# Kernel tuning notes

Measured on AMD Instinct MI355X. Metric: run time of the kernel, lower is better.

The kernel has to match this reference:

```python
import jax, jax.numpy as jnp
import numpy as np

N = 1_000_000
B = 64            # number of point clouds (segments)
IN_DIM = 3
HID = 128
AFF = 16
AH = 64           # agent hidden
AL = 32           # agent latent
AA = 8            # agent action


def setup_inputs() -> dict:
    key = jax.random.key(0)
    ks = jax.random.split(key, 20)
    s = 0.05
    inp = {
        "pos": jax.random.normal(ks[0], (N, IN_DIM), jnp.float32),
        "batch": jnp.sort(jax.random.randint(ks[1], (N,), 0, B, jnp.int32)),
        "agent_h": jnp.zeros((B, AH), jnp.float32),
        "coherence_signal_prev": jnp.zeros((B, 1), jnp.float32),
        "coherence_spatial_prev": jnp.zeros((N,), jnp.float32),
        # FunctorF params (3 -> 128 -> 16)
        "Wf1": jax.random.normal(ks[2], (IN_DIM, HID), jnp.float32) * s,
        "bf1": jnp.zeros((HID,), jnp.float32),
        "Wf2": jax.random.normal(ks[3], (HID, AFF), jnp.float32) * s,
        "bf2": jnp.zeros((AFF,), jnp.float32),
        # FunctorG params (16 -> 128 -> 3)
        "Wg1": jax.random.normal(ks[4], (AFF, HID), jnp.float32) * s,
        "bg1": jnp.zeros((HID,), jnp.float32),
        "Wg2": jax.random.normal(ks[5], (HID, IN_DIM), jnp.float32) * s,
        "bg2": jnp.zeros((IN_DIM,), jnp.float32),
        # AgentC GRU cell (obs=16 -> h=64) + latent/action heads
        "Wx": jax.random.normal(ks[6], (AFF, 3 * AH), jnp.float32) * s,
        "Wh": jax.random.normal(ks[7], (AH, 3 * AH), jnp.float32) * s,
        "bx": jnp.zeros((3 * AH,), jnp.float32),
        "bh": jnp.zeros((3 * AH,), jnp.float32),
        "Wlat": jax.random.normal(ks[8], (AH, AL), jnp.float32) * s,
        "blat": jnp.zeros((AL,), jnp.float32),
        "Wact": jax.random.normal(ks[9], (AL, AA), jnp.float32) * s,
        "bact": jnp.zeros((AA,), jnp.float32),
    }
    return inp


def _segment_mean(x, seg, num_segments):
    # x: (N, ...) float; seg: (N,) int. Mean over each segment (empty -> 0).
    sums = jax.ops.segment_sum(x, seg, num_segments=num_segments)
    counts = jax.ops.segment_sum(jnp.ones_like(seg, x.dtype), seg, num_segments=num_segments)
    denom = jnp.maximum(counts, 1.0)
    return sums / (denom[:, None] if x.ndim > 1 else denom)


def _forward(pos, batch, agent_h, Wf1, bf1, Wf2, bf2, Wg1, bg1, Wg2, bg2,
             Wx, Wh, bx, bh, Wlat, blat, Wact, bact):
    # F: Shape -> Affordance (per-point MLP)
    affordances = jax.nn.relu(pos @ Wf1 + bf1) @ Wf2 + bf2              # (N, AFF)
    # G: Affordance -> Shape reconstruction
    reconstructed_pos = jax.nn.relu(affordances @ Wg1 + bg1) @ Wg2 + bg2  # (N, 3)
    # Coherence (eta): per-point squared error, segment-mean per cloud
    point_errors = jnp.sum((pos - reconstructed_pos) ** 2, axis=-1)     # (N,)
    coherence_signal = _segment_mean(point_errors, batch, B)[:, None]   # (B, 1)
    coherence_spatial = point_errors                                    # (N,)
    # Segment-mean pooled affordances per cloud
    batch_affordances = _segment_mean(affordances, batch, B)            # (B, AFF)
    # AgentC: GRU cell + latent/action heads
    gx = batch_affordances @ Wx + bx                                    # (B, 3*AH)
    gh = agent_h @ Wh + bh                                              # (B, 3*AH)
    gx_r, gx_z, gx_n = jnp.split(gx, 3, axis=-1)
    gh_r, gh_z, gh_n = jnp.split(gh, 3, axis=-1)
    r = jax.nn.sigmoid(gx_r + gh_r)
    z = jax.nn.sigmoid(gx_z + gh_z)
    n = jnp.tanh(gx_n + r * gh_n)
    agent_h_next = (1.0 - z) * n + z * agent_h                          # (B, AH)
    latent = jnp.tanh(agent_h_next @ Wlat + blat)                       # (B, AL)
    agent_action = latent @ Wact + bact                                 # (B, AA)
    return (affordances, reconstructed_pos, coherence_signal,
            coherence_spatial, agent_action, agent_h_next)


def reference(pos, batch, agent_h, coherence_signal_prev, coherence_spatial_prev,
              Wf1, bf1, Wf2, bf2, Wg1, bg1, Wg2, bg2,
              Wx, Wh, bx, bh, Wlat, blat, Wact, bact):
    # coherence_*_prev are part of the original interface but unused in the math.
    return _forward(pos, batch, agent_h, Wf1, bf1, Wf2, bf2, Wg1, bg1, Wg2, bg2,
                    Wx, Wh, bx, bh, Wlat, blat, Wact, bact)
```

## Files before the change

kernel.cpp:

```cpp
#include <hip/hip_runtime.h>
#include <stdint.h>

#define N_PTS 1000000
#define B_SEG 64
#define HID 128
#define AFFD 16
#define AH 64
#define AL 32
#define AA 8

#define TPB 256
#define NT 8
#define PTS_WAVE (16 * NT)
#define PTS_BLK (PTS_WAVE * 4)
#define MAX_REP 8

#define O_AFF 0
#define O_REC (16 * N_PTS)
#define O_SIG (19 * N_PTS)
#define O_SPA (19 * N_PTS + B_SEG)
#define O_ACT (20 * N_PTS + B_SEG)
#define O_HN  (20 * N_PTS + B_SEG + B_SEG * AA)


typedef __attribute__((ext_vector_type(8))) short bf16x8;
typedef __attribute__((ext_vector_type(4))) float f32x4;

static __device__ __forceinline__ short f2bf(float f) {
  __bf16 b = (__bf16)f;
  return __builtin_bit_cast(short, b);
}

__global__ __launch_bounds__(TPB, 1) void point_kernel(
    const float* __restrict__ pos, const int* __restrict__ batch,
    const float* __restrict__ Wf1, const float* __restrict__ bf1v,
    const float* __restrict__ Wf2, const float* __restrict__ bf2v,
    const float* __restrict__ Wg1, const float* __restrict__ bg1v,
    const float* __restrict__ Wg2, const float* __restrict__ bg2v,
    float* __restrict__ out, float* __restrict__ ws, int rep) {
  const int lane = threadIdx.x & 63;
  const int wid = threadIdx.x >> 6;
  const int m = lane & 15;
  const int q = lane >> 4;
  const int wbase = blockIdx.x * PTS_BLK + wid * PTS_WAVE;
  float* __restrict__ wsr = ws + (size_t)(blockIdx.x % rep) * (B_SEG * 18);

  bf16x8 Af1[8], Ag1[8], Af2[4], Ag2[4];
#pragma unroll
  for (int jb = 0; jb < 8; jb++) {
    const int j = jb * 16 + m;
    bf16x8 a = {0, 0, 0, 0, 0, 0, 0, 0};
    if (q == 0) {
      a[0] = f2bf(Wf1[0 * HID + j]);
      a[1] = f2bf(Wf1[1 * HID + j]);
      a[2] = f2bf(Wf1[2 * HID + j]);
      a[3] = f2bf(bf1v[j]);
    }
    Af1[jb] = a;
    bf16x8 g = {0, 0, 0, 0, 0, 0, 0, 0};
#pragma unroll
    for (int e = 0; e < 4; e++) g[e] = f2bf(Wg1[(4 * q + e) * HID + j]);
    if (q == 0) g[4] = f2bf(bg1v[j]);
    Ag1[jb] = g;
  }
#pragma unroll
  for (int kb = 0; kb < 4; kb++) {
    bf16x8 a2, g2;
#pragma unroll
    for (int e = 0; e < 8; e++) {
      const int j = kb * 32 + 4 * q + (e & 3) + 16 * (e >> 2);
      a2[e] = f2bf(Wf2[j * AFFD + m]);
      g2[e] = (m < 3) ? f2bf(Wg2[j * 3 + m]) : (short)0;
    }
    Af2[kb] = a2;
    Ag2[kb] = g2;
  }
  const float bf2r0 = bf2v[4 * q + 0], bf2r1 = bf2v[4 * q + 1];
  const float bf2r2 = bf2v[4 * q + 2], bf2r3 = bf2v[4 * q + 3];
  const float bg20 = bg2v[0], bg21 = bg2v[1], bg22 = bg2v[2];
  const short one = (short)0x3F80;
  const f32x4 zf = {0.f, 0.f, 0.f, 0.f};

  int cur = -1, cntT = 0;
  float acc0 = 0.f, acc1 = 0.f, acc2 = 0.f, acc3 = 0.f, accE = 0.f;

  auto flush = [&]() {
    float r0 = acc0, r1 = acc1, r2 = acc2, r3 = acc3, re = accE;
#pragma unroll
    for (int msk = 1; msk <= 8; msk <<= 1) {
      r0 += __shfl_xor(r0, msk);
      r1 += __shfl_xor(r1, msk);
      r2 += __shfl_xor(r2, msk);
      r3 += __shfl_xor(r3, msk);
      re += __shfl_xor(re, msk);
    }
    if (m == 0) {
      float* wp = wsr + cur * 18;
      atomicAdd(wp + 2 + 4 * q + 0, r0);
      atomicAdd(wp + 2 + 4 * q + 1, r1);
      atomicAdd(wp + 2 + 4 * q + 2, r2);
      atomicAdd(wp + 2 + 4 * q + 3, r3);
      if (q == 0) {
        atomicAdd(wp + 0, re);
        atomicAdd(wp + 1, 16.f * (float)cntT);
      }
    }
    acc0 = acc1 = acc2 = acc3 = accE = 0.f;
    cntT = 0;
  };

  auto do_pair = [&](int pt0, float (&aa)[2][4], float (&ee)[2], int (&sgv)[2],
                     bool (&vv)[2]) {
    float X[2], Y[2], Z[2];
    bf16x8 Bp[2];
#pragma unroll
    for (int u = 0; u < 2; u++) {
      const int p = pt0 + 16 * u + m;
      vv[u] = (p < N_PTS);
      const int pc = vv[u] ? p : (N_PTS - 1);
      X[u] = pos[pc * 3 + 0];
      Y[u] = pos[pc * 3 + 1];
      Z[u] = pos[pc * 3 + 2];
      sgv[u] = batch[pc];
      bf16x8 b = {0, 0, 0, 0, 0, 0, 0, 0};
      if (q == 0) {
        b[0] = f2bf(X[u]);
        b[1] = f2bf(Y[u]);
        b[2] = f2bf(Z[u]);
        b[3] = one;
      }
      Bp[u] = b;
    }

    bf16x8 Bh[2][4];
#pragma unroll
    for (int u = 0; u < 2; u++)
#pragma unroll
      for (int kb = 0; kb < 4; kb++) {
        f32x4 c0 = __builtin_amdgcn_mfma_f32_16x16x32_bf16(Af1[2 * kb + 0], Bp[u], zf, 0, 0, 0);
        f32x4 c1 = __builtin_amdgcn_mfma_f32_16x16x32_bf16(Af1[2 * kb + 1], Bp[u], zf, 0, 0, 0);
        bf16x8 b;
        b[0] = f2bf(fmaxf(c0[0], 0.f));
        b[1] = f2bf(fmaxf(c0[1], 0.f));
        b[2] = f2bf(fmaxf(c0[2], 0.f));
        b[3] = f2bf(fmaxf(c0[3], 0.f));
        b[4] = f2bf(fmaxf(c1[0], 0.f));
        b[5] = f2bf(fmaxf(c1[1], 0.f));
        b[6] = f2bf(fmaxf(c1[2], 0.f));
        b[7] = f2bf(fmaxf(c1[3], 0.f));
        Bh[u][kb] = b;
      }

    bf16x8 Ba[2];
#pragma unroll
    for (int u = 0; u < 2; u++) {
      f32x4 c01 = __builtin_amdgcn_mfma_f32_16x16x32_bf16(Af2[0], Bh[u][0], zf, 0, 0, 0);
      c01 = __builtin_amdgcn_mfma_f32_16x16x32_bf16(Af2[1], Bh[u][1], c01, 0, 0, 0);
      f32x4 c23 = __builtin_amdgcn_mfma_f32_16x16x32_bf16(Af2[2], Bh[u][2], zf, 0, 0, 0);
      c23 = __builtin_amdgcn_mfma_f32_16x16x32_bf16(Af2[3], Bh[u][3], c23, 0, 0, 0);
      aa[u][0] = c01[0] + c23[0] + bf2r0;
      aa[u][1] = c01[1] + c23[1] + bf2r1;
      aa[u][2] = c01[2] + c23[2] + bf2r2;
      aa[u][3] = c01[3] + c23[3] + bf2r3;
      bf16x8 b;
      b[0] = f2bf(aa[u][0]);
      b[1] = f2bf(aa[u][1]);
      b[2] = f2bf(aa[u][2]);
      b[3] = f2bf(aa[u][3]);
      b[4] = one;
      b[5] = 0;
      b[6] = 0;
      b[7] = 0;
      Ba[u] = b;
    }

    bf16x8 Bh2[2][4];
#pragma unroll
    for (int u = 0; u < 2; u++)
#pragma unroll
      for (int kb = 0; kb < 4; kb++) {
        f32x4 c0 = __builtin_amdgcn_mfma_f32_16x16x32_bf16(Ag1[2 * kb + 0], Ba[u], zf, 0, 0, 0);
        f32x4 c1 = __builtin_amdgcn_mfma_f32_16x16x32_bf16(Ag1[2 * kb + 1], Ba[u], zf, 0, 0, 0);
        bf16x8 b;
        b[0] = f2bf(fmaxf(c0[0], 0.f));
        b[1] = f2bf(fmaxf(c0[1], 0.f));
        b[2] = f2bf(fmaxf(c0[2], 0.f));
        b[3] = f2bf(fmaxf(c0[3], 0.f));
        b[4] = f2bf(fmaxf(c1[0], 0.f));
        b[5] = f2bf(fmaxf(c1[1], 0.f));
        b[6] = f2bf(fmaxf(c1[2], 0.f));
        b[7] = f2bf(fmaxf(c1[3], 0.f));
        Bh2[u][kb] = b;
      }

#pragma unroll
    for (int u = 0; u < 2; u++) {
      f32x4 c01 = __builtin_amdgcn_mfma_f32_16x16x32_bf16(Ag2[0], Bh2[u][0], zf, 0, 0, 0);
      c01 = __builtin_amdgcn_mfma_f32_16x16x32_bf16(Ag2[1], Bh2[u][1], c01, 0, 0, 0);
      f32x4 c23 = __builtin_amdgcn_mfma_f32_16x16x32_bf16(Ag2[2], Bh2[u][2], zf, 0, 0, 0);
      c23 = __builtin_amdgcn_mfma_f32_16x16x32_bf16(Ag2[3], Bh2[u][3], c23, 0, 0, 0);

      float err = 0.f, rc0 = 0.f, rc1 = 0.f, rc2 = 0.f;
      if (q == 0) {
        rc0 = c01[0] + c23[0] + bg20;
        rc1 = c01[1] + c23[1] + bg21;
        rc2 = c01[2] + c23[2] + bg22;
        const float dx = X[u] - rc0, dy = Y[u] - rc1, dz = Z[u] - rc2;
        err = fmaf(dx, dx, fmaf(dy, dy, dz * dz));
      }
      ee[u] = err;

      if (vv[u]) {
        const int p = pt0 + 16 * u + m;
        float4 st;
        st.x = aa[u][0]; st.y = aa[u][1]; st.z = aa[u][2]; st.w = aa[u][3];
        *(float4*)(out + O_AFF + (size_t)p * 16 + 4 * q) = st;
        if (q == 0) {
          float* orc = out + O_REC + (size_t)p * 3;
          orc[0] = rc0; orc[1] = rc1; orc[2] = rc2;
          out[O_SPA + p] = err;
        }
      }
    }
  };

  const int cA = (wbase < N_PTS) ? wbase : (N_PTS - 1);
  const int cB = (wbase + PTS_WAVE - 1 < N_PTS) ? (wbase + PTS_WAVE - 1) : (N_PTS - 1);
  const int segFirst = batch[cA];
  const bool wave_clean = (wbase + PTS_WAVE <= N_PTS) && (segFirst == batch[cB]);

  float aa[2][4];
  float ee[2];
  int sgv[2];
  bool vv[2];

  if (wave_clean) {
#pragma unroll 1
    for (int tt = 0; tt < NT; tt += 2) {
      do_pair(wbase + tt * 16, aa, ee, sgv, vv);
      acc0 += aa[0][0] + aa[1][0];
      acc1 += aa[0][1] + aa[1][1];
      acc2 += aa[0][2] + aa[1][2];
      acc3 += aa[0][3] + aa[1][3];
      accE += ee[0] + ee[1];
    }
    cur = segFirst;
    cntT = NT;
    flush();
  } else {
#pragma unroll 1
    for (int tt = 0; tt < NT; tt += 2) {
      do_pair(wbase + tt * 16, aa, ee, sgv, vv);
#pragma unroll
      for (int u = 0; u < 2; u++) {
        const int pt0u = wbase + (tt + u) * 16;
        const int useg = __shfl(sgv[u], 0);
        const bool cln = __all(sgv[u] == useg) && (pt0u + 16 <= N_PTS);
        if (cln && useg == cur) {
          acc0 += aa[u][0]; acc1 += aa[u][1];
          acc2 += aa[u][2]; acc3 += aa[u][3];
          accE += ee[u];
          cntT++;
        } else {
          if (cntT > 0) flush();
          if (cln) {
            cur = useg;
            acc0 = aa[u][0]; acc1 = aa[u][1];
            acc2 = aa[u][2]; acc3 = aa[u][3];
            accE = ee[u];
            cntT = 1;
          } else {
            cur = -1;
            if (vv[u]) {
              float* wp = wsr + sgv[u] * 18;
              atomicAdd(wp + 2 + 4 * q + 0, aa[u][0]);
              atomicAdd(wp + 2 + 4 * q + 1, aa[u][1]);
              atomicAdd(wp + 2 + 4 * q + 2, aa[u][2]);
              atomicAdd(wp + 2 + 4 * q + 3, aa[u][3]);
              if (q == 0) {
                atomicAdd(wp + 0, ee[u]);
                atomicAdd(wp + 1, 1.f);
              }
            }
          }
        }
      }
    }
    if (cntT > 0) flush();
  }
}

__global__ __launch_bounds__(64) void agent_kernel(
    const float* __restrict__ ws, int rep, const float* __restrict__ agent_h,
    const float* __restrict__ Wx, const float* __restrict__ Wh,
    const float* __restrict__ bx, const float* __restrict__ bh,
    const float* __restrict__ Wlat, const float* __restrict__ blat,
    const float* __restrict__ Wact, const float* __restrict__ bact,
    float* __restrict__ out) {
  const int b = blockIdx.x;
  const int t = threadIdx.x;
  __shared__ float sAff[AFFD];
  __shared__ float sHn[AH];
  __shared__ float sLat[AL];

  float errs = 0.f, cnts = 0.f, affs = 0.f;
  for (int r = 0; r < rep; r++) {
    const float* wp = ws + ((size_t)r * B_SEG + b) * 18;
    errs += wp[0];
    cnts += wp[1];
    if (t < AFFD) affs += wp[2 + t];
  }
  const float cnt = fmaxf(cnts, 1.f);
  if (t == 0) out[O_SIG + b] = errs / cnt;
  if (t < AFFD) sAff[t] = affs / cnt;
  const float h_prev = agent_h[b * AH + t];
  __syncthreads();

  float pr  = bx[t] + bh[t];
  float pz  = bx[64 + t] + bh[64 + t];
  float pnx = bx[128 + t];
  float pnh = bh[128 + t];
#pragma unroll
  for (int k = 0; k < AFFD; k++) {
    const float a = sAff[k];
    pr  = fmaf(a, Wx[k * 192 + t], pr);
    pz  = fmaf(a, Wx[k * 192 + 64 + t], pz);
    pnx = fmaf(a, Wx[k * 192 + 128 + t], pnx);
  }
#pragma unroll
  for (int k = 0; k < AH; k++) {
    const float h = __shfl(h_prev, k);
    pr  = fmaf(h, Wh[k * 192 + t], pr);
    pz  = fmaf(h, Wh[k * 192 + 64 + t], pz);
    pnh = fmaf(h, Wh[k * 192 + 128 + t], pnh);
  }
  const float r = 1.f / (1.f + expf(-pr));
  const float z = 1.f / (1.f + expf(-pz));
  const float n = tanhf(pnx + r * pnh);
  const float hn = fmaf(1.f - z, n, z * h_prev);
  sHn[t] = hn;
  out[O_HN + b * AH + t] = hn;
  __syncthreads();

  if (t < AL) {
    float acc = blat[t];
#pragma unroll
    for (int k = 0; k < AH; k++) acc = fmaf(sHn[k], Wlat[k * AL + t], acc);
    sLat[t] = tanhf(acc);
  }
  __syncthreads();

  if (t < AA) {
    float acc = bact[t];
#pragma unroll
    for (int k = 0; k < AL; k++) acc = fmaf(sLat[k], Wact[k * AA + t], acc);
    out[O_ACT + b * AA + t] = acc;
  }
}

extern "C" void kernel_launch(void* const* d_in, const int* in_sizes, int n_in,
                              void* d_out, int out_size, void* d_ws, size_t ws_size,
                              hipStream_t stream) {
  const float* pos     = (const float*)d_in[0];
  const int*   batch   = (const int*)d_in[1];
  const float* agent_h = (const float*)d_in[2];
  const float* Wf1  = (const float*)d_in[5];
  const float* bf1v = (const float*)d_in[6];
  const float* Wf2  = (const float*)d_in[7];
  const float* bf2v = (const float*)d_in[8];
  const float* Wg1  = (const float*)d_in[9];
  const float* bg1v = (const float*)d_in[10];
  const float* Wg2  = (const float*)d_in[11];
  const float* bg2v = (const float*)d_in[12];
  const float* Wx   = (const float*)d_in[13];
  const float* Wh   = (const float*)d_in[14];
  const float* bx   = (const float*)d_in[15];
  const float* bh   = (const float*)d_in[16];
  const float* Wlat = (const float*)d_in[17];
  const float* blat = (const float*)d_in[18];
  const float* Wact = (const float*)d_in[19];
  const float* bact = (const float*)d_in[20];
  float* out = (float*)d_out;
  float* ws = (float*)d_ws;

  const size_t one_rep = (size_t)B_SEG * 18 * sizeof(float);
  int rep = (int)(ws_size / one_rep);
  if (rep > MAX_REP) rep = MAX_REP;
  if (rep < 1) rep = 1;

  hipMemsetAsync(ws, 0, (size_t)rep * one_rep, stream);

  const int nblk = (N_PTS + PTS_BLK - 1) / PTS_BLK;
  point_kernel<<<nblk, TPB, 0, stream>>>(pos, batch, Wf1, bf1v, Wf2, bf2v,
                                         Wg1, bg1v, Wg2, bg2v, out, ws, rep);
  agent_kernel<<<B_SEG, 64, 0, stream>>>(ws, rep, agent_h, Wx, Wh, bx, bh,
                                         Wlat, blat, Wact, bact, out);
}
```

Measured before the change: 228.4 us.

## Add unrolled clean-wave path with register double-buffered position prefetch

For waves whose points all belong to one segment, a dedicated fully unrolled path now prefetches the next pair of point positions into a second register buffer while the current pair runs through the MFMA chain. It also skips the per-point batch loads and segment checks on that path. The launch bound is raised to allow two blocks per CU, which tightens the register budget. The extra prefetch registers and full unrolling under that tighter budget risk spills.

```diff
diff --git a/kernel.cpp b/kernel.cpp
--- a/kernel.cpp
+++ b/kernel.cpp
@@ -31,7 +31,7 @@
   return __builtin_bit_cast(short, b);
 }
 
-__global__ __launch_bounds__(TPB, 1) void point_kernel(
+__global__ __launch_bounds__(TPB, 2) void point_kernel(
     const float* __restrict__ pos, const int* __restrict__ batch,
     const float* __restrict__ Wf1, const float* __restrict__ bf1v,
     const float* __restrict__ Wf2, const float* __restrict__ bf2v,
@@ -108,6 +108,147 @@
     acc0 = acc1 = acc2 = acc3 = accE = 0.f;
     cntT = 0;
   };
+
+  const int cA = (wbase < N_PTS) ? wbase : (N_PTS - 1);
+  const int cB = (wbase + PTS_WAVE - 1 < N_PTS) ? (wbase + PTS_WAVE - 1) : (N_PTS - 1);
+  const int segFirst = batch[cA];
+  const bool wave_clean = (wbase + PTS_WAVE <= N_PTS) && (segFirst == batch[cB]);
+
+  if (wave_clean) {
+    float Xb[2][2], Yb[2][2], Zb[2][2];
+#pragma unroll
+    for (int u = 0; u < 2; u++) {
+      const int p = wbase + 16 * u + m;
+      Xb[0][u] = pos[p * 3 + 0];
+      Yb[0][u] = pos[p * 3 + 1];
+      Zb[0][u] = pos[p * 3 + 2];
+    }
+
+#pragma unroll
+    for (int pp = 0; pp < NT / 2; pp++) {
+      const int cr = pp & 1, nx = cr ^ 1;
+      if (pp + 1 < NT / 2) {
+#pragma unroll
+        for (int u = 0; u < 2; u++) {
+          const int p = wbase + (pp + 1) * 32 + 16 * u + m;
+          Xb[nx][u] = pos[p * 3 + 0];
+          Yb[nx][u] = pos[p * 3 + 1];
+          Zb[nx][u] = pos[p * 3 + 2];
+        }
+      }
+
+      bf16x8 Bp[2];
+#pragma unroll
+      for (int u = 0; u < 2; u++) {
+        bf16x8 b = {0, 0, 0, 0, 0, 0, 0, 0};
+        if (q == 0) {
+          b[0] = f2bf(Xb[cr][u]);
+          b[1] = f2bf(Yb[cr][u]);
+          b[2] = f2bf(Zb[cr][u]);
+          b[3] = one;
+        }
+        Bp[u] = b;
+      }
+
+      bf16x8 Bh[2][4];
+#pragma unroll
+      for (int u = 0; u < 2; u++)
+#pragma unroll
+        for (int kb = 0; kb < 4; kb++) {
+          f32x4 c0 = __builtin_amdgcn_mfma_f32_16x16x32_bf16(Af1[2 * kb + 0], Bp[u], zf, 0, 0, 0);
+          f32x4 c1 = __builtin_amdgcn_mfma_f32_16x16x32_bf16(Af1[2 * kb + 1], Bp[u], zf, 0, 0, 0);
+          bf16x8 b;
+          b[0] = f2bf(fmaxf(c0[0], 0.f));
+          b[1] = f2bf(fmaxf(c0[1], 0.f));
+          b[2] = f2bf(fmaxf(c0[2], 0.f));
+          b[3] = f2bf(fmaxf(c0[3], 0.f));
+          b[4] = f2bf(fmaxf(c1[0], 0.f));
+          b[5] = f2bf(fmaxf(c1[1], 0.f));
+          b[6] = f2bf(fmaxf(c1[2], 0.f));
+          b[7] = f2bf(fmaxf(c1[3], 0.f));
+          Bh[u][kb] = b;
+        }
+
+      float aa[2][4];
+      bf16x8 Ba[2];
+#pragma unroll
+      for (int u = 0; u < 2; u++) {
+        f32x4 c01 = __builtin_amdgcn_mfma_f32_16x16x32_bf16(Af2[0], Bh[u][0], zf, 0, 0, 0);
+        c01 = __builtin_amdgcn_mfma_f32_16x16x32_bf16(Af2[1], Bh[u][1], c01, 0, 0, 0);
+        f32x4 c23 = __builtin_amdgcn_mfma_f32_16x16x32_bf16(Af2[2], Bh[u][2], zf, 0, 0, 0);
+        c23 = __builtin_amdgcn_mfma_f32_16x16x32_bf16(Af2[3], Bh[u][3], c23, 0, 0, 0);
+        aa[u][0] = c01[0] + c23[0] + bf2r0;
+        aa[u][1] = c01[1] + c23[1] + bf2r1;
+        aa[u][2] = c01[2] + c23[2] + bf2r2;
+        aa[u][3] = c01[3] + c23[3] + bf2r3;
+        bf16x8 b;
+        b[0] = f2bf(aa[u][0]);
+        b[1] = f2bf(aa[u][1]);
+        b[2] = f2bf(aa[u][2]);
+        b[3] = f2bf(aa[u][3]);
+        b[4] = one;
+        b[5] = 0;
+        b[6] = 0;
+        b[7] = 0;
+        Ba[u] = b;
+      }
+
+      bf16x8 Bh2[2][4];
+#pragma unroll
+      for (int u = 0; u < 2; u++)
+#pragma unroll
+        for (int kb = 0; kb < 4; kb++) {
+          f32x4 c0 = __builtin_amdgcn_mfma_f32_16x16x32_bf16(Ag1[2 * kb + 0], Ba[u], zf, 0, 0, 0);
+          f32x4 c1 = __builtin_amdgcn_mfma_f32_16x16x32_bf16(Ag1[2 * kb + 1], Ba[u], zf, 0, 0, 0);
+          bf16x8 b;
+          b[0] = f2bf(fmaxf(c0[0], 0.f));
+          b[1] = f2bf(fmaxf(c0[1], 0.f));
+          b[2] = f2bf(fmaxf(c0[2], 0.f));
+          b[3] = f2bf(fmaxf(c0[3], 0.f));
+          b[4] = f2bf(fmaxf(c1[0], 0.f));
+          b[5] = f2bf(fmaxf(c1[1], 0.f));
+          b[6] = f2bf(fmaxf(c1[2], 0.f));
+          b[7] = f2bf(fmaxf(c1[3], 0.f));
+          Bh2[u][kb] = b;
+        }
+
+#pragma unroll
+      for (int u = 0; u < 2; u++) {
+        f32x4 c01 = __builtin_amdgcn_mfma_f32_16x16x32_bf16(Ag2[0], Bh2[u][0], zf, 0, 0, 0);
+        c01 = __builtin_amdgcn_mfma_f32_16x16x32_bf16(Ag2[1], Bh2[u][1], c01, 0, 0, 0);
+        f32x4 c23 = __builtin_amdgcn_mfma_f32_16x16x32_bf16(Ag2[2], Bh2[u][2], zf, 0, 0, 0);
+        c23 = __builtin_amdgcn_mfma_f32_16x16x32_bf16(Ag2[3], Bh2[u][3], c23, 0, 0, 0);
+
+        float err = 0.f, rc0 = 0.f, rc1 = 0.f, rc2 = 0.f;
+        if (q == 0) {
+          rc0 = c01[0] + c23[0] + bg20;
+          rc1 = c01[1] + c23[1] + bg21;
+          rc2 = c01[2] + c23[2] + bg22;
+          const float dx = Xb[cr][u] - rc0, dy = Yb[cr][u] - rc1, dz = Zb[cr][u] - rc2;
+          err = fmaf(dx, dx, fmaf(dy, dy, dz * dz));
+        }
+        acc0 += aa[u][0];
+        acc1 += aa[u][1];
+        acc2 += aa[u][2];
+        acc3 += aa[u][3];
+        accE += err;
+
+        const int p = wbase + pp * 32 + 16 * u + m;
+        float4 st;
+        st.x = aa[u][0]; st.y = aa[u][1]; st.z = aa[u][2]; st.w = aa[u][3];
+        *(float4*)(out + O_AFF + (size_t)p * 16 + 4 * q) = st;
+        if (q == 0) {
+          float* orc = out + O_REC + (size_t)p * 3;
+          orc[0] = rc0; orc[1] = rc1; orc[2] = rc2;
+          out[O_SPA + p] = err;
+        }
+      }
+    }
+    cur = segFirst;
+    cntT = NT;
+    flush();
+    return;
+  }
 
   auto do_pair = [&](int pt0, float (&aa)[2][4], float (&ee)[2], int (&sgv)[2],
                      bool (&vv)[2]) {
@@ -224,70 +365,49 @@
     }
   };
 
-  const int cA = (wbase < N_PTS) ? wbase : (N_PTS - 1);
-  const int cB = (wbase + PTS_WAVE - 1 < N_PTS) ? (wbase + PTS_WAVE - 1) : (N_PTS - 1);
-  const int segFirst = batch[cA];
-  const bool wave_clean = (wbase + PTS_WAVE <= N_PTS) && (segFirst == batch[cB]);
-
   float aa[2][4];
   float ee[2];
   int sgv[2];
   bool vv[2];
-
-  if (wave_clean) {
 #pragma unroll 1
-    for (int tt = 0; tt < NT; tt += 2) {
-      do_pair(wbase + tt * 16, aa, ee, sgv, vv);
-      acc0 += aa[0][0] + aa[1][0];
-      acc1 += aa[0][1] + aa[1][1];
-      acc2 += aa[0][2] + aa[1][2];
-      acc3 += aa[0][3] + aa[1][3];
-      accE += ee[0] + ee[1];
-    }
-    cur = segFirst;
-    cntT = NT;
-    flush();
-  } else {
-#pragma unroll 1
-    for (int tt = 0; tt < NT; tt += 2) {
-      do_pair(wbase + tt * 16, aa, ee, sgv, vv);
-#pragma unroll
-      for (int u = 0; u < 2; u++) {
-        const int pt0u = wbase + (tt + u) * 16;
-        const int useg = __shfl(sgv[u], 0);
-        const bool cln = __all(sgv[u] == useg) && (pt0u + 16 <= N_PTS);
-        if (cln && useg == cur) {
-          acc0 += aa[u][0]; acc1 += aa[u][1];
-          acc2 += aa[u][2]; acc3 += aa[u][3];
-          accE += ee[u];
-          cntT++;
+  for (int tt = 0; tt < NT; tt += 2) {
+    do_pair(wbase + tt * 16, aa, ee, sgv, vv);
+#pragma unroll
+    for (int u = 0; u < 2; u++) {
+      const int pt0u = wbase + (tt + u) * 16;
+      const int useg = __shfl(sgv[u], 0);
+      const bool cln = __all(sgv[u] == useg) && (pt0u + 16 <= N_PTS);
+      if (cln && useg == cur) {
+        acc0 += aa[u][0]; acc1 += aa[u][1];
+        acc2 += aa[u][2]; acc3 += aa[u][3];
+        accE += ee[u];
+        cntT++;
+      } else {
+        if (cntT > 0) flush();
+        if (cln) {
+          cur = useg;
+          acc0 = aa[u][0]; acc1 = aa[u][1];
+          acc2 = aa[u][2]; acc3 = aa[u][3];
+          accE = ee[u];
+          cntT = 1;
         } else {
-          if (cntT > 0) flush();
-          if (cln) {
-            cur = useg;
-            acc0 = aa[u][0]; acc1 = aa[u][1];
-            acc2 = aa[u][2]; acc3 = aa[u][3];
-            accE = ee[u];
-            cntT = 1;
-          } else {
-            cur = -1;
-            if (vv[u]) {
-              float* wp = wsr + sgv[u] * 18;
-              atomicAdd(wp + 2 + 4 * q + 0, aa[u][0]);
-              atomicAdd(wp + 2 + 4 * q + 1, aa[u][1]);
-              atomicAdd(wp + 2 + 4 * q + 2, aa[u][2]);
-              atomicAdd(wp + 2 + 4 * q + 3, aa[u][3]);
-              if (q == 0) {
-                atomicAdd(wp + 0, ee[u]);
-                atomicAdd(wp + 1, 1.f);
-              }
+          cur = -1;
+          if (vv[u]) {
+            float* wp = wsr + sgv[u] * 18;
+            atomicAdd(wp + 2 + 4 * q + 0, aa[u][0]);
+            atomicAdd(wp + 2 + 4 * q + 1, aa[u][1]);
+            atomicAdd(wp + 2 + 4 * q + 2, aa[u][2]);
+            atomicAdd(wp + 2 + 4 * q + 3, aa[u][3]);
+            if (q == 0) {
+              atomicAdd(wp + 0, ee[u]);
+              atomicAdd(wp + 1, 1.f);
             }
           }
         }
       }
     }
-    if (cntT > 0) flush();
-  }
+  }
+  if (cntT > 0) flush();
 }
 
 __global__ __launch_bounds__(64) void agent_kernel(
```

Measured after the change: 210.1 us. 1.09x faster.

## Use single-wave blocks and software-prefetch next point pair positions

Applied to the files above, without the earlier changes.

Shrinks the point kernel to one wave per block (64 threads, launch bounds allowing two blocks) so each block covers 128 points. It restructures the per-pair loop to load the next pair's positions into registers while the current pair's MFMA chain runs. It also skips reading the batch index on clean waves by loading it only in the mixed-segment path. The aim is to hide global load latency and balance work better, at the cost of more blocks and extra registers for the prefetch buffers.

```diff
diff --git a/kernel.cpp b/kernel.cpp
--- a/kernel.cpp
+++ b/kernel.cpp
@@ -9,10 +9,10 @@
 #define AL 32
 #define AA 8
 
-#define TPB 256
+#define TPB 64
 #define NT 8
 #define PTS_WAVE (16 * NT)
-#define PTS_BLK (PTS_WAVE * 4)
+#define PTS_BLK PTS_WAVE
 #define MAX_REP 8
 
 #define O_AFF 0
@@ -31,7 +31,7 @@
   return __builtin_bit_cast(short, b);
 }
 
-__global__ __launch_bounds__(TPB, 1) void point_kernel(
+__global__ __launch_bounds__(TPB, 2) void point_kernel(
     const float* __restrict__ pos, const int* __restrict__ batch,
     const float* __restrict__ Wf1, const float* __restrict__ bf1v,
     const float* __restrict__ Wf2, const float* __restrict__ bf2v,
@@ -39,10 +39,9 @@
     const float* __restrict__ Wg2, const float* __restrict__ bg2v,
     float* __restrict__ out, float* __restrict__ ws, int rep) {
   const int lane = threadIdx.x & 63;
-  const int wid = threadIdx.x >> 6;
   const int m = lane & 15;
   const int q = lane >> 4;
-  const int wbase = blockIdx.x * PTS_BLK + wid * PTS_WAVE;
+  const int wbase = blockIdx.x * PTS_BLK;
   float* __restrict__ wsr = ws + (size_t)(blockIdx.x % rep) * (B_SEG * 18);
 
   bf16x8 Af1[8], Ag1[8], Af2[4], Ag2[4];
@@ -109,24 +108,42 @@
     cntT = 0;
   };
 
-  auto do_pair = [&](int pt0, float (&aa)[2][4], float (&ee)[2], int (&sgv)[2],
-                     bool (&vv)[2]) {
-    float X[2], Y[2], Z[2];
+  const int cA = (wbase < N_PTS) ? wbase : (N_PTS - 1);
+  const int cB = (wbase + PTS_WAVE - 1 < N_PTS) ? (wbase + PTS_WAVE - 1) : (N_PTS - 1);
+  const int segFirst = batch[cA];
+  const bool wave_clean = (wbase + PTS_WAVE <= N_PTS) && (segFirst == batch[cB]);
+
+  float cX[2], cY[2], cZ[2], nX[2], nY[2], nZ[2];
+#pragma unroll
+  for (int u = 0; u < 2; u++) {
+    int p = wbase + 16 * u + m;
+    if (p >= N_PTS) p = N_PTS - 1;
+    cX[u] = pos[p * 3 + 0];
+    cY[u] = pos[p * 3 + 1];
+    cZ[u] = pos[p * 3 + 2];
+  }
+
+#pragma unroll 1
+  for (int pp = 0; pp < NT / 2; pp++) {
+    if (pp + 1 < NT / 2) {
+#pragma unroll
+      for (int u = 0; u < 2; u++) {
+        int p = wbase + (pp + 1) * 32 + 16 * u + m;
+        if (p >= N_PTS) p = N_PTS - 1;
+        nX[u] = pos[p * 3 + 0];
+        nY[u] = pos[p * 3 + 1];
+        nZ[u] = pos[p * 3 + 2];
+      }
+    }
+
     bf16x8 Bp[2];
 #pragma unroll
     for (int u = 0; u < 2; u++) {
-      const int p = pt0 + 16 * u + m;
-      vv[u] = (p < N_PTS);
-      const int pc = vv[u] ? p : (N_PTS - 1);
-      X[u] = pos[pc * 3 + 0];
-      Y[u] = pos[pc * 3 + 1];
-      Z[u] = pos[pc * 3 + 2];
-      sgv[u] = batch[pc];
       bf16x8 b = {0, 0, 0, 0, 0, 0, 0, 0};
       if (q == 0) {
-        b[0] = f2bf(X[u]);
-        b[1] = f2bf(Y[u]);
-        b[2] = f2bf(Z[u]);
+        b[0] = f2bf(cX[u]);
+        b[1] = f2bf(cY[u]);
+        b[2] = f2bf(cZ[u]);
         b[3] = one;
       }
       Bp[u] = b;
@@ -151,6 +168,7 @@
         Bh[u][kb] = b;
       }
 
+    float aa[2][4];
     bf16x8 Ba[2];
 #pragma unroll
     for (int u = 0; u < 2; u++) {
@@ -193,6 +211,7 @@
         Bh2[u][kb] = b;
       }
 
+    float ee[2];
 #pragma unroll
     for (int u = 0; u < 2; u++) {
       f32x4 c01 = __builtin_amdgcn_mfma_f32_16x16x32_bf16(Ag2[0], Bh2[u][0], zf, 0, 0, 0);
@@ -205,13 +224,13 @@
         rc0 = c01[0] + c23[0] + bg20;
         rc1 = c01[1] + c23[1] + bg21;
         rc2 = c01[2] + c23[2] + bg22;
-        const float dx = X[u] - rc0, dy = Y[u] - rc1, dz = Z[u] - rc2;
+        const float dx = cX[u] - rc0, dy = cY[u] - rc1, dz = cZ[u] - rc2;
         err = fmaf(dx, dx, fmaf(dy, dy, dz * dz));
       }
       ee[u] = err;
 
-      if (vv[u]) {
-        const int p = pt0 + 16 * u + m;
+      const int p = wbase + pp * 32 + 16 * u + m;
+      if (p < N_PTS) {
         float4 st;
         st.x = aa[u][0]; st.y = aa[u][1]; st.z = aa[u][2]; st.w = aa[u][3];
         *(float4*)(out + O_AFF + (size_t)p * 16 + 4 * q) = st;
@@ -222,40 +241,23 @@
         }
       }
     }
-  };
-
-  const int cA = (wbase < N_PTS) ? wbase : (N_PTS - 1);
-  const int cB = (wbase + PTS_WAVE - 1 < N_PTS) ? (wbase + PTS_WAVE - 1) : (N_PTS - 1);
-  const int segFirst = batch[cA];
-  const bool wave_clean = (wbase + PTS_WAVE <= N_PTS) && (segFirst == batch[cB]);
-
-  float aa[2][4];
-  float ee[2];
-  int sgv[2];
-  bool vv[2];
-
-  if (wave_clean) {
-#pragma unroll 1
-    for (int tt = 0; tt < NT; tt += 2) {
-      do_pair(wbase + tt * 16, aa, ee, sgv, vv);
+
+    if (wave_clean) {
       acc0 += aa[0][0] + aa[1][0];
       acc1 += aa[0][1] + aa[1][1];
       acc2 += aa[0][2] + aa[1][2];
       acc3 += aa[0][3] + aa[1][3];
       accE += ee[0] + ee[1];
-    }
-    cur = segFirst;
-    cntT = NT;
-    flush();
-  } else {
-#pragma unroll 1
-    for (int tt = 0; tt < NT; tt += 2) {
-      do_pair(wbase + tt * 16, aa, ee, sgv, vv);
+    } else {
 #pragma unroll
       for (int u = 0; u < 2; u++) {
-        const int pt0u = wbase + (tt + u) * 16;
-        const int useg = __shfl(sgv[u], 0);
-        const bool cln = __all(sgv[u] == useg) && (pt0u + 16 <= N_PTS);
+        const int pt0u = wbase + pp * 32 + 16 * u;
+        int p = pt0u + m;
+        const bool v = (p < N_PTS);
+        if (p >= N_PTS) p = N_PTS - 1;
+        const int sg = batch[p];
+        const int useg = __shfl(sg, 0);
+        const bool cln = __all(sg == useg) && (pt0u + 16 <= N_PTS);
         if (cln && useg == cur) {
           acc0 += aa[u][0]; acc1 += aa[u][1];
           acc2 += aa[u][2]; acc3 += aa[u][3];
@@ -271,8 +273,8 @@
             cntT = 1;
           } else {
             cur = -1;
-            if (vv[u]) {
-              float* wp = wsr + sgv[u] * 18;
+            if (v) {
+              float* wp = wsr + sg * 18;
               atomicAdd(wp + 2 + 4 * q + 0, aa[u][0]);
               atomicAdd(wp + 2 + 4 * q + 1, aa[u][1]);
               atomicAdd(wp + 2 + 4 * q + 2, aa[u][2]);
@@ -286,7 +288,21 @@
         }
       }
     }
-    if (cntT > 0) flush();
+
+#pragma unroll
+    for (int u = 0; u < 2; u++) {
+      cX[u] = nX[u];
+      cY[u] = nY[u];
+      cZ[u] = nZ[u];
+    }
+  }
+
+  if (wave_clean) {
+    cur = segFirst;
+    cntT = NT;
+    flush();
+  } else if (cntT > 0) {
+    flush();
   }
 }
 
```

After: 216.3 us. 1.06x faster.
